# Optimization experiments

Hardware: AMD Instinct MI355X
Metric: run time of the kernel (lower is better)

## Reference

```python
import jax, jax.numpy as jnp
import numpy as np

A, H, HI = 4, 3, 2  # nagents, n_pol_heads, n_intr_rew_heads (sep_extr_head=True)
# leave-one-out index table: row i lists all agents k != i, in ascending order (torch loop order)
LOO = np.array([[k for k in range(A) if k != i] for i in range(A)])  # [A, A-1]


def setup_inputs() -> dict:
    key = jax.random.key(0)
    ks = jax.random.split(key, 12)
    B, S, C, D = 32768, 256, 16, 128  # batch, vect_state_size, action_size, hidden_dim
    IN = C * (A - 1) + D  # 176 critic input dim
    r = lambda k, shp, s=0.05: jax.random.normal(k, shp, dtype=jnp.float32) * s
    return {
        "state_vect": jax.random.normal(ks[0], (B, S), dtype=jnp.float32),
        "acs": jax.random.normal(ks[1], (A, H, B, C), dtype=jnp.float32),
        "enc_W": r(ks[2], (S, D)),
        "enc_b": r(ks[3], (D,)),
        "extr_W1": r(ks[4], (H, A, IN, D)),
        "extr_b1": r(ks[5], (H, A, D)),
        "extr_W2": r(ks[6], (H, A, D, C)),
        "extr_b2": r(ks[7], (H, A, C)),
        "intr_W1": r(ks[8], (HI, A, IN, D)),
        "intr_b1": r(ks[9], (HI, A, D)),
        "intr_W2": r(ks[10], (HI, A, D, C)),
        "intr_b2": r(ks[11], (HI, A, C)),
    }


def reference(state_vect, acs, enc_W, enc_b, extr_W1, extr_b1, extr_W2, extr_b2,
              intr_W1, intr_b1, intr_W2, intr_b2):
    B, C = acs.shape[2], acs.shape[3]
    D = enc_W.shape[1]
    # shared state encoder: Linear -> ReLU
    enc = jax.nn.relu(state_vect @ enc_W + enc_b)  # [B, D]
    # leave-one-out action concat per (agent, head): cat(acs[k!=i, j]) ++ enc
    rel = acs[LOO]                                 # [A, A-1, H, B, C]
    rel = rel.transpose(0, 2, 3, 1, 4).reshape(A, H, B, (A - 1) * C)
    x = jnp.concatenate([rel, jnp.broadcast_to(enc, (A, H, B, D))], axis=-1)  # [A,H,B,IN]
    # greedy action index of agent i's own head-j policy output
    int_acs = jnp.argmax(acs, axis=-1)             # [A, H, B]

    def critic(xin, W1, b1, W2, b2):
        # xin: [A, Hc, B, IN]; W1: [Hc, A, IN, D]; W2: [Hc, A, D, C]
        h = jax.nn.relu(jnp.einsum('ahbi,haid->ahbd', xin, W1)
                        + b1.transpose(1, 0, 2)[:, :, None, :])
        return (jnp.einsum('ahbd,hadc->ahbc', h, W2)
                + b2.transpose(1, 0, 2)[:, :, None, :])  # [A, Hc, B, C]

    extr_all_q = critic(x, extr_W1, extr_b1, extr_W2, extr_b2)          # [A,H,B,C]
    extr_q = jnp.take_along_axis(extr_all_q, int_acs[..., None], axis=-1)  # [A,H,B,1]
    # intr critics exist only for heads j>=1 (sep_extr_head=True -> offset -1)
    intr_all_q = critic(x[:, 1:], intr_W1, intr_b1, intr_W2, intr_b2)   # [A,HI,B,C]
    intr_q = jnp.take_along_axis(intr_all_q, int_acs[:, 1:, :, None], axis=-1)  # [A,HI,B,1]
    return extr_q, intr_q
```

## Files before the change

kernel.cpp:

```cpp
#include <hip/hip_runtime.h>

#define NA 4
#define NH 3
#define NHI 2
#define Bsz 32768
#define Ssz 256
#define Csz 16
#define Dsz 128
#define INsz 176
#define NP 20
#define KP 192
#define GT 2

typedef __bf16 v8bf __attribute__((ext_vector_type(8)));
typedef float v4f __attribute__((ext_vector_type(4)));

#define OFF_ENC    0
#define OFF_ACSBF  8388608
#define OFF_W1F    20971520
#define OFF_ENCWF  21954560
#define OFF_W2T    22020096
#define OFF_AMX    22102016
#define OFF_ZERO   22495232

#define N_ACSROW (NA*NH*Bsz)
#define N_W1F   (NP*192*32)
#define N_ENCWF (256*32)
#define N_W2T   (NP*Csz*Dsz)
#define N_ZERO  16
#define N_PREP  (N_ACSROW+N_W1F+N_ENCWF+N_W2T+N_ZERO)

__global__ __launch_bounds__(256) void prep_kernel(
    const float* __restrict__ acs, const float* __restrict__ encW,
    const float* __restrict__ eW1, const float* __restrict__ iW1,
    const float* __restrict__ eW2, const float* __restrict__ iW2,
    char* __restrict__ ws)
{
    long tid = (long)blockIdx.x * 256 + threadIdx.x;

    if (tid < N_ACSROW) {
        const float4* src = (const float4*)(acs + (size_t)tid * 16);
        float4 f0 = src[0], f1 = src[1], f2 = src[2], f3 = src[3];
        float v[16] = {f0.x,f0.y,f0.z,f0.w, f1.x,f1.y,f1.z,f1.w,
                       f2.x,f2.y,f2.z,f2.w, f3.x,f3.y,f3.z,f3.w};
        v8bf o0, o1;
        #pragma unroll
        for (int i = 0; i < 8; ++i) { o0[i] = (__bf16)v[i]; o1[i] = (__bf16)v[8 + i]; }
        v8bf* dst = (v8bf*)(ws + OFF_ACSBF) + tid * 2;
        dst[0] = o0; dst[1] = o1;
        float best = v[0]; int bi = 0;
        #pragma unroll
        for (int c = 1; c < 16; ++c) if (v[c] > best) { best = v[c]; bi = c; }
        ((unsigned char*)(ws + OFF_AMX))[tid] = (unsigned char)bi;
        return;
    }
    tid -= N_ACSROW;
    if (tid < N_W1F) {
        const int n4 = (int)(tid & 31) * 4;
        const int k  = (int)((tid >> 5) % 192);
        const int p  = (int)(tid / 6144);
        const float* W1;
        if (p < 12) { int ai = p / 3, hj = p % 3; W1 = eW1 + (size_t)(hj * NA + ai) * INsz * Dsz; }
        else { int qq = p - 12; int ai = qq >> 1, jj = qq & 1; W1 = iW1 + (size_t)(jj * NA + ai) * INsz * Dsz; }
        float4 f = (k < INsz) ? *(const float4*)(W1 + (size_t)k * Dsz + n4)
                              : (float4){0.f, 0.f, 0.f, 0.f};
        const int kc = k >> 5, q = (k >> 3) & 3, j = k & 7;
        __bf16* dst = (__bf16*)(ws + OFF_W1F);
        const float fv[4] = {f.x, f.y, f.z, f.w};
        #pragma unroll
        for (int i = 0; i < 4; ++i) {
            const int n = n4 + i, nt = n >> 4, m = n & 15;
            dst[((size_t)(p * 6 + kc) * 8 + nt) * 512 + (q * 16 + m) * 8 + j] = (__bf16)fv[i];
        }
        return;
    }
    tid -= N_W1F;
    if (tid < N_ENCWF) {
        const int n4 = (int)(tid & 31) * 4;
        const int k  = (int)(tid >> 5);
        float4 f = *(const float4*)(encW + (size_t)k * Dsz + n4);
        const int kc = k >> 5, q = (k >> 3) & 3, j = k & 7;
        __bf16* dst = (__bf16*)(ws + OFF_ENCWF);
        const float fv[4] = {f.x, f.y, f.z, f.w};
        #pragma unroll
        for (int i = 0; i < 4; ++i) {
            const int n = n4 + i, nt = n >> 4, m = n & 15;
            dst[((size_t)kc * 8 + nt) * 512 + (q * 16 + m) * 8 + j] = (__bf16)fv[i];
        }
        return;
    }
    tid -= N_ENCWF;
    if (tid < N_W2T) {
        int d = (int)(tid & 127);
        int rest = (int)(tid >> 7);
        int c = rest & 15, p = rest >> 4;
        const float* W2;
        if (p < 12) { int ai = p / 3, hj = p % 3; W2 = eW2 + (size_t)(hj * NA + ai) * Dsz * Csz; }
        else { int qq = p - 12; int ai = qq >> 1, jj = qq & 1; W2 = iW2 + (size_t)(jj * NA + ai) * Dsz * Csz; }
        ((__bf16*)(ws + OFF_W2T))[(size_t)p * 2048 + c * 128 + (d & 15) * 8 + (d >> 4)]
            = (__bf16)W2[(size_t)d * Csz + c];
        return;
    }
    tid -= N_W2T;
    if (tid < N_ZERO) ((float*)(ws + OFF_ZERO))[tid] = 0.f;
}

__global__ __launch_bounds__(256) void enc_kernel(const float* __restrict__ sv,
                                                  const float* __restrict__ encb,
                                                  char* __restrict__ ws)
{
    __shared__ __bf16 tb[4][16 * 136];

    const int t = threadIdx.x;
    const int wv = t >> 6, lane = t & 63, m = lane & 15, q = lane >> 4;
    const int R = blockIdx.x * 64 + wv * 16 + m;
    const __bf16* encwf = (const __bf16*)(ws + OFF_ENCWF);
    char* enct = ws + OFF_ENC;

    v4f acc[8];
    #pragma unroll
    for (int nt = 0; nt < 8; ++nt) acc[nt] = (v4f){0.f, 0.f, 0.f, 0.f};

    const float* arow = sv + (size_t)R * Ssz + q * 8;
    #pragma unroll
    for (int kc = 0; kc < 8; ++kc) {
        float4 f0 = *(const float4*)(arow + kc * 32);
        float4 f1 = *(const float4*)(arow + kc * 32 + 4);
        v8bf af;
        af[0]=(__bf16)f0.x; af[1]=(__bf16)f0.y; af[2]=(__bf16)f0.z; af[3]=(__bf16)f0.w;
        af[4]=(__bf16)f1.x; af[5]=(__bf16)f1.y; af[6]=(__bf16)f1.z; af[7]=(__bf16)f1.w;
        #pragma unroll
        for (int nt = 0; nt < 8; ++nt) {
            v8bf bf = *(const v8bf*)(encwf + ((size_t)kc * 8 + nt) * 512 + lane * 8);
            acc[nt] = __builtin_amdgcn_mfma_f32_16x16x32_bf16(af, bf, acc[nt], 0, 0, 0);
        }
    }
    #pragma unroll
    for (int nt = 0; nt < 8; ++nt) {
        const float bias = encb[nt * 16 + m];
        #pragma unroll
        for (int rg = 0; rg < 4; ++rg) {
            float v = acc[nt][rg] + bias;
            v = v > 0.f ? v : 0.f;
            tb[wv][(q * 4 + rg) * 136 + nt * 16 + m] = (__bf16)v;
        }
    }
    __syncthreads();
    const int rt = blockIdx.x * 4 + wv;
    #pragma unroll
    for (int kc = 0; kc < 4; ++kc) {
        v8bf v = *(const v8bf*)&tb[wv][m * 136 + kc * 32 + q * 8];
        *(v8bf*)(enct + ((size_t)(rt * 4 + kc) * 64 + lane) * 16) = v;
    }
}

#define LD_AF(D, KC, GG) \
  { _Pragma("unroll") \
    for (int mt_ = 0; mt_ < 4; ++mt_) \
      D[mt_] = *(const v8bf*)(base[KC] + (size_t)((mt_ + 16 * (GG)) * strd[KC])); }

#define MFMA_KC(AF, KC) \
  { _Pragma("unroll") \
    for (int nt_ = 0; nt_ < 8; ++nt_) { \
      v8bf bf_ = *(const v8bf*)&w1s[(size_t)(((KC) * 8 + nt_) * 512) + lane * 8]; \
      acc[0][nt_] = __builtin_amdgcn_mfma_f32_16x16x32_bf16(AF[0], bf_, acc[0][nt_], 0, 0, 0); \
      acc[1][nt_] = __builtin_amdgcn_mfma_f32_16x16x32_bf16(AF[1], bf_, acc[1][nt_], 0, 0, 0); \
      acc[2][nt_] = __builtin_amdgcn_mfma_f32_16x16x32_bf16(AF[2], bf_, acc[2][nt_], 0, 0, 0); \
      acc[3][nt_] = __builtin_amdgcn_mfma_f32_16x16x32_bf16(AF[3], bf_, acc[3][nt_], 0, 0, 0); \
    } }

__global__ __launch_bounds__(256, 2) void critic_kernel(
    const float* __restrict__ eb1, const float* __restrict__ eb2,
    const float* __restrict__ ib1, const float* __restrict__ ib2,
    const char* __restrict__ ws, float* __restrict__ out)
{
    __shared__ __bf16 w1s[6 * 8 * 512];
    __shared__ __bf16 w2s[16 * 136];

    const int t = threadIdx.x;
    const int p  = blockIdx.y;
    const int rb = blockIdx.x;
    const int wv = t >> 6, lane = t & 63, m = lane & 15, q = lane >> 4;

    int ai, hj;
    const float *b1, *b2;
    float* outp;
    if (p < 12) {
        ai = p / 3; hj = p % 3;
        const int wi = hj * NA + ai;
        b1 = eb1 + (size_t)wi * Dsz; b2 = eb2 + (size_t)wi * Csz;
        outp = out + (size_t)(ai * NH + hj) * Bsz;
    } else {
        const int qq = p - 12; ai = qq >> 1; const int jj = qq & 1; hj = jj + 1;
        const int wi = jj * NA + ai;
        b1 = ib1 + (size_t)wi * Dsz; b2 = ib2 + (size_t)wi * Csz;
        outp = out + (size_t)NA * NH * Bsz + (size_t)(ai * NHI + jj) * Bsz;
    }

    const char* acsb = ws + OFF_ACSBF;
    const char* enct = ws + OFF_ENC;
    const __bf16* w1f = (const __bf16*)(ws + OFF_W1F) + (size_t)p * 6 * 8 * 512;
    const __bf16* w2t = (const __bf16*)(ws + OFF_W2T) + (size_t)p * 2048;
    const unsigned char* amxp = (const unsigned char*)(ws + OFF_AMX)
        + (size_t)(ai * NH + hj) * Bsz + (size_t)rb * 512 + wv * 64;
    const char* zerop = ws + OFF_ZERO;

    {
        const v8bf* src = (const v8bf*)w1f;
        #pragma unroll
        for (int i = 0; i < 12; ++i)
            ((v8bf*)w1s)[i * 256 + t] = src[i * 256 + t];
        v8bf wv2 = ((const v8bf*)w2t)[t];
        *(v8bf*)&w2s[(t >> 4) * 136 + (t & 15) * 8] = wv2;
    }

    const int loo0 = 0 + (0 >= ai), loo1 = 1 + (1 >= ai), loo2 = 2 + (2 >= ai);
    const size_t rowoff = ((size_t)rb * 512 + wv * 64 + m) * 32;
    const char* pl0 = acsb + (size_t)(loo0 * NH + hj) * Bsz * 32 + rowoff;
    const char* pl1 = acsb + (size_t)(loo1 * NH + hj) * Bsz * 32 + rowoff;
    const char* pl2 = acsb + (size_t)(loo2 * NH + hj) * Bsz * 32 + rowoff;
    const int rt0 = rb * 32 + wv * 4;
    const char* encB = enct + (size_t)rt0 * 4096 + m * 16;

    const char* base[6];
    int strd[6];
    base[0] = (q < 2) ? (pl0 + q * 16) : (pl1 + (q - 2) * 16);           strd[0] = 512;
    base[1] = (q < 2) ? (pl2 + q * 16) : (encB + (q - 2) * 256);         strd[1] = (q < 2) ? 512 : 4096;
    base[2] = encB + (q + 2)  * 256;                                     strd[2] = 4096;
    base[3] = encB + (q + 6)  * 256;                                     strd[3] = 4096;
    base[4] = encB + (q + 10) * 256;                                     strd[4] = 4096;
    base[5] = (q < 2) ? (encB + (14 + q) * 256) : zerop;                 strd[5] = (q < 2) ? 4096 : 0;

    float b1v[8];
    #pragma unroll
    for (int nt = 0; nt < 8; ++nt) b1v[nt] = b1[nt * 16 + m];

    v4f acc[4][8];
    #pragma unroll
    for (int i = 0; i < 4; ++i)
        #pragma unroll
        for (int j = 0; j < 8; ++j)
            acc[i][j] = (v4f){0.f, 0.f, 0.f, 0.f};

    v8bf afA[4], afB[4];
    LD_AF(afA, 0, 0)

    __syncthreads();

    #pragma unroll
    for (int g = 0; g < GT; ++g) {
        unsigned int cw[4];
        #pragma unroll
        for (int mt = 0; mt < 4; ++mt)
            cw[mt] = *(const unsigned int*)(amxp + g * 256 + mt * 16 + q * 4);

        LD_AF(afB, 1, g)  MFMA_KC(afA, 0)
        LD_AF(afA, 2, g)  MFMA_KC(afB, 1)
        LD_AF(afB, 3, g)  MFMA_KC(afA, 2)
        LD_AF(afA, 4, g)  MFMA_KC(afB, 3)
        LD_AF(afB, 5, g)  MFMA_KC(afA, 4)
        if (g + 1 < GT) { LD_AF(afA, 0, g + 1) }
        MFMA_KC(afB, 5)

        #pragma unroll
        for (int mt = 0; mt < 4; ++mt) {
            const unsigned int cwv = cw[mt];
            #pragma unroll
            for (int rg = 0; rg < 4; ++rg) {
                const int c = (cwv >> (8 * rg)) & 255;
                const v8bf w2v = *(const v8bf*)&w2s[c * 136 + m * 8];
                float partial = 0.f;
                #pragma unroll
                for (int nt = 0; nt < 8; ++nt) {
                    float h = acc[mt][nt][rg] + b1v[nt];
                    h = h > 0.f ? h : 0.f;
                    partial += h * (float)w2v[nt];
                }
                partial += __shfl_xor(partial, 1, 64);
                partial += __shfl_xor(partial, 2, 64);
                partial += __shfl_xor(partial, 4, 64);
                partial += __shfl_xor(partial, 8, 64);
                if (m == 0)
                    outp[(size_t)rb * 512 + g * 256 + wv * 64 + mt * 16 + q * 4 + rg]
                        = partial + b2[c];
            }
            if (g + 1 < GT) {
                #pragma unroll
                for (int nt = 0; nt < 8; ++nt) acc[mt][nt] = (v4f){0.f, 0.f, 0.f, 0.f};
            }
        }
    }
}

extern "C" void kernel_launch(void* const* d_in, const int* in_sizes, int n_in,
                              void* d_out, int out_size, void* d_ws, size_t ws_size,
                              hipStream_t stream) {
    const float* sv   = (const float*)d_in[0];
    const float* acs  = (const float*)d_in[1];
    const float* encW = (const float*)d_in[2];
    const float* encb = (const float*)d_in[3];
    const float* eW1  = (const float*)d_in[4];
    const float* eb1  = (const float*)d_in[5];
    const float* eW2  = (const float*)d_in[6];
    const float* eb2  = (const float*)d_in[7];
    const float* iW1  = (const float*)d_in[8];
    const float* ib1  = (const float*)d_in[9];
    const float* iW2  = (const float*)d_in[10];
    const float* ib2  = (const float*)d_in[11];
    float* out = (float*)d_out;
    char* ws = (char*)d_ws;

    hipLaunchKernelGGL(prep_kernel, dim3((N_PREP + 255) / 256), dim3(256), 0, stream,
                       acs, encW, eW1, iW1, eW2, iW2, ws);
    hipLaunchKernelGGL(enc_kernel, dim3(Bsz / 64), dim3(256), 0, stream, sv, encb, ws);
    hipLaunchKernelGGL(critic_kernel, dim3(Bsz / 512, NP), dim3(256), 0, stream,
                       eb1, eb2, ib1, ib2, ws, out);
}
```

Baseline: 170.5 us.

## Fold b1 into padded GEMM K and transpose MFMA to cut epilogue shuffles

The first-layer bias b1 is folded into the padded K dimension of the packed W1, with a constant-one bf16 entry placed in the zero region, so the epilogue no longer adds it. The MFMA operands are swapped so each lane holds one batch row across the hidden dimension. The second-layer reduction then needs two cross-lane shuffles per row tile instead of four per register group. W2 is stored in shared memory with an XOR swizzle by action index to avoid bank conflicts. Bias rounding to bf16 slightly changes numerics.

```diff
diff --git a/kernel.cpp b/kernel.cpp
--- a/kernel.cpp
+++ b/kernel.cpp
@@ -34,6 +34,7 @@
     const float* __restrict__ acs, const float* __restrict__ encW,
     const float* __restrict__ eW1, const float* __restrict__ iW1,
     const float* __restrict__ eW2, const float* __restrict__ iW2,
+    const float* __restrict__ eb1, const float* __restrict__ ib1,
     char* __restrict__ ws)
 {
     long tid = (long)blockIdx.x * 256 + threadIdx.x;
@@ -59,11 +60,15 @@
         const int n4 = (int)(tid & 31) * 4;
         const int k  = (int)((tid >> 5) % 192);
         const int p  = (int)(tid / 6144);
-        const float* W1;
-        if (p < 12) { int ai = p / 3, hj = p % 3; W1 = eW1 + (size_t)(hj * NA + ai) * INsz * Dsz; }
-        else { int qq = p - 12; int ai = qq >> 1, jj = qq & 1; W1 = iW1 + (size_t)(jj * NA + ai) * INsz * Dsz; }
-        float4 f = (k < INsz) ? *(const float4*)(W1 + (size_t)k * Dsz + n4)
-                              : (float4){0.f, 0.f, 0.f, 0.f};
+        const float* W1; const float* B1;
+        if (p < 12) { int ai = p / 3, hj = p % 3; int wi = hj * NA + ai;
+                      W1 = eW1 + (size_t)wi * INsz * Dsz; B1 = eb1 + (size_t)wi * Dsz; }
+        else { int qq = p - 12; int ai = qq >> 1, jj = qq & 1; int wi = jj * NA + ai;
+               W1 = iW1 + (size_t)wi * INsz * Dsz; B1 = ib1 + (size_t)wi * Dsz; }
+        float4 f;
+        if (k < INsz)       f = *(const float4*)(W1 + (size_t)k * Dsz + n4);
+        else if (k == INsz) f = *(const float4*)(B1 + n4);
+        else                f = (float4){0.f, 0.f, 0.f, 0.f};
         const int kc = k >> 5, q = (k >> 3) & 3, j = k & 7;
         __bf16* dst = (__bf16*)(ws + OFF_W1F);
         const float fv[4] = {f.x, f.y, f.z, f.w};
@@ -97,12 +102,15 @@
         const float* W2;
         if (p < 12) { int ai = p / 3, hj = p % 3; W2 = eW2 + (size_t)(hj * NA + ai) * Dsz * Csz; }
         else { int qq = p - 12; int ai = qq >> 1, jj = qq & 1; W2 = iW2 + (size_t)(jj * NA + ai) * Dsz * Csz; }
-        ((__bf16*)(ws + OFF_W2T))[(size_t)p * 2048 + c * 128 + (d & 15) * 8 + (d >> 4)]
+        const int dlow = d & 15, dt = d >> 4;
+        ((__bf16*)(ws + OFF_W2T))[(size_t)p * 2048 + c * 128 + ((dlow ^ c) * 8) + dt]
             = (__bf16)W2[(size_t)d * Csz + c];
         return;
     }
     tid -= N_W2T;
-    if (tid < N_ZERO) ((float*)(ws + OFF_ZERO))[tid] = 0.f;
+    if (tid < N_ZERO) {
+        ((unsigned int*)(ws + OFF_ZERO))[tid] = (tid == 0) ? 0x00003F80u : 0u;
+    }
 }
 
 __global__ __launch_bounds__(256) void enc_kernel(const float* __restrict__ sv,
@@ -163,19 +171,18 @@
   { _Pragma("unroll") \
     for (int nt_ = 0; nt_ < 8; ++nt_) { \
       v8bf bf_ = *(const v8bf*)&w1s[(size_t)(((KC) * 8 + nt_) * 512) + lane * 8]; \
-      acc[0][nt_] = __builtin_amdgcn_mfma_f32_16x16x32_bf16(AF[0], bf_, acc[0][nt_], 0, 0, 0); \
-      acc[1][nt_] = __builtin_amdgcn_mfma_f32_16x16x32_bf16(AF[1], bf_, acc[1][nt_], 0, 0, 0); \
-      acc[2][nt_] = __builtin_amdgcn_mfma_f32_16x16x32_bf16(AF[2], bf_, acc[2][nt_], 0, 0, 0); \
-      acc[3][nt_] = __builtin_amdgcn_mfma_f32_16x16x32_bf16(AF[3], bf_, acc[3][nt_], 0, 0, 0); \
+      acc[0][nt_] = __builtin_amdgcn_mfma_f32_16x16x32_bf16(bf_, AF[0], acc[0][nt_], 0, 0, 0); \
+      acc[1][nt_] = __builtin_amdgcn_mfma_f32_16x16x32_bf16(bf_, AF[1], acc[1][nt_], 0, 0, 0); \
+      acc[2][nt_] = __builtin_amdgcn_mfma_f32_16x16x32_bf16(bf_, AF[2], acc[2][nt_], 0, 0, 0); \
+      acc[3][nt_] = __builtin_amdgcn_mfma_f32_16x16x32_bf16(bf_, AF[3], acc[3][nt_], 0, 0, 0); \
     } }
 
 __global__ __launch_bounds__(256, 2) void critic_kernel(
-    const float* __restrict__ eb1, const float* __restrict__ eb2,
-    const float* __restrict__ ib1, const float* __restrict__ ib2,
+    const float* __restrict__ eb2, const float* __restrict__ ib2,
     const char* __restrict__ ws, float* __restrict__ out)
 {
     __shared__ __bf16 w1s[6 * 8 * 512];
-    __shared__ __bf16 w2s[16 * 136];
+    __shared__ __bf16 w2s[16 * 128];
 
     const int t = threadIdx.x;
     const int p  = blockIdx.y;
@@ -183,17 +190,15 @@
     const int wv = t >> 6, lane = t & 63, m = lane & 15, q = lane >> 4;
 
     int ai, hj;
-    const float *b1, *b2;
+    const float* b2;
     float* outp;
     if (p < 12) {
         ai = p / 3; hj = p % 3;
-        const int wi = hj * NA + ai;
-        b1 = eb1 + (size_t)wi * Dsz; b2 = eb2 + (size_t)wi * Csz;
+        b2 = eb2 + (size_t)(hj * NA + ai) * Csz;
         outp = out + (size_t)(ai * NH + hj) * Bsz;
     } else {
         const int qq = p - 12; ai = qq >> 1; const int jj = qq & 1; hj = jj + 1;
-        const int wi = jj * NA + ai;
-        b1 = ib1 + (size_t)wi * Dsz; b2 = ib2 + (size_t)wi * Csz;
+        b2 = ib2 + (size_t)(jj * NA + ai) * Csz;
         outp = out + (size_t)NA * NH * Bsz + (size_t)(ai * NHI + jj) * Bsz;
     }
 
@@ -210,8 +215,7 @@
         #pragma unroll
         for (int i = 0; i < 12; ++i)
             ((v8bf*)w1s)[i * 256 + t] = src[i * 256 + t];
-        v8bf wv2 = ((const v8bf*)w2t)[t];
-        *(v8bf*)&w2s[(t >> 4) * 136 + (t & 15) * 8] = wv2;
+        ((v8bf*)w2s)[t] = ((const v8bf*)w2t)[t];
     }
 
     const int loo0 = 0 + (0 >= ai), loo1 = 1 + (1 >= ai), loo2 = 2 + (2 >= ai);
@@ -229,11 +233,8 @@
     base[2] = encB + (q + 2)  * 256;                                     strd[2] = 4096;
     base[3] = encB + (q + 6)  * 256;                                     strd[3] = 4096;
     base[4] = encB + (q + 10) * 256;                                     strd[4] = 4096;
-    base[5] = (q < 2) ? (encB + (14 + q) * 256) : zerop;                 strd[5] = (q < 2) ? 4096 : 0;
-
-    float b1v[8];
-    #pragma unroll
-    for (int nt = 0; nt < 8; ++nt) b1v[nt] = b1[nt * 16 + m];
+    base[5] = (q < 2) ? (encB + (14 + q) * 256) : (zerop + (q - 2) * 16);
+    strd[5] = (q < 2) ? 4096 : 0;
 
     v4f acc[4][8];
     #pragma unroll
@@ -249,10 +250,10 @@
 
     #pragma unroll
     for (int g = 0; g < GT; ++g) {
-        unsigned int cw[4];
+        int cb[4];
         #pragma unroll
         for (int mt = 0; mt < 4; ++mt)
-            cw[mt] = *(const unsigned int*)(amxp + g * 256 + mt * 16 + q * 4);
+            cb[mt] = amxp[g * 256 + mt * 16 + m];
 
         LD_AF(afB, 1, g)  MFMA_KC(afA, 0)
         LD_AF(afA, 2, g)  MFMA_KC(afB, 1)
@@ -264,26 +265,25 @@
 
         #pragma unroll
         for (int mt = 0; mt < 4; ++mt) {
-            const unsigned int cwv = cw[mt];
+            const int c = cb[mt];
+            const v8bf wv0 = *(const v8bf*)&w2s[c * 128 + ((q * 4 + 0) ^ c) * 8];
+            const v8bf wv1 = *(const v8bf*)&w2s[c * 128 + ((q * 4 + 1) ^ c) * 8];
+            const v8bf wv2 = *(const v8bf*)&w2s[c * 128 + ((q * 4 + 2) ^ c) * 8];
+            const v8bf wv3 = *(const v8bf*)&w2s[c * 128 + ((q * 4 + 3) ^ c) * 8];
+            float s0 = 0.f, s1 = 0.f, s2 = 0.f, s3 = 0.f;
             #pragma unroll
-            for (int rg = 0; rg < 4; ++rg) {
-                const int c = (cwv >> (8 * rg)) & 255;
-                const v8bf w2v = *(const v8bf*)&w2s[c * 136 + m * 8];
-                float partial = 0.f;
-                #pragma unroll
-                for (int nt = 0; nt < 8; ++nt) {
-                    float h = acc[mt][nt][rg] + b1v[nt];
-                    h = h > 0.f ? h : 0.f;
-                    partial += h * (float)w2v[nt];
-                }
-                partial += __shfl_xor(partial, 1, 64);
-                partial += __shfl_xor(partial, 2, 64);
-                partial += __shfl_xor(partial, 4, 64);
-                partial += __shfl_xor(partial, 8, 64);
-                if (m == 0)
-                    outp[(size_t)rb * 512 + g * 256 + wv * 64 + mt * 16 + q * 4 + rg]
-                        = partial + b2[c];
+            for (int nt = 0; nt < 8; ++nt) {
+                const v4f z = acc[mt][nt];
+                s0 += fmaxf(z[0], 0.f) * (float)wv0[nt];
+                s1 += fmaxf(z[1], 0.f) * (float)wv1[nt];
+                s2 += fmaxf(z[2], 0.f) * (float)wv2[nt];
+                s3 += fmaxf(z[3], 0.f) * (float)wv3[nt];
             }
+            float tsum = (s0 + s1) + (s2 + s3);
+            tsum += __shfl_xor(tsum, 16, 64);
+            tsum += __shfl_xor(tsum, 32, 64);
+            if (q == 0)
+                outp[(size_t)rb * 512 + g * 256 + wv * 64 + mt * 16 + m] = tsum + b2[c];
             if (g + 1 < GT) {
                 #pragma unroll
                 for (int nt = 0; nt < 8; ++nt) acc[mt][nt] = (v4f){0.f, 0.f, 0.f, 0.f};
@@ -311,8 +311,8 @@
     char* ws = (char*)d_ws;
 
     hipLaunchKernelGGL(prep_kernel, dim3((N_PREP + 255) / 256), dim3(256), 0, stream,
-                       acs, encW, eW1, iW1, eW2, iW2, ws);
+                       acs, encW, eW1, iW1, eW2, iW2, eb1, ib1, ws);
     hipLaunchKernelGGL(enc_kernel, dim3(Bsz / 64), dim3(256), 0, stream, sv, encb, ws);
     hipLaunchKernelGGL(critic_kernel, dim3(Bsz / 512, NP), dim3(256), 0, stream,
-                       eb1, eb2, ib1, ib2, ws, out);
+                       eb2, ib2, ws, out);
 }
```

New measurement: 162.6 us. 1.05x faster.
